# Performance work log

Hardware: AMD Instinct MI355X
Metric: run time of the kernel (lower is better)

## Reference

```python
import jax, jax.numpy as jnp
import numpy as np

B = 131072
UNITS = 256
INPUT_DIM = 256


def setup_inputs() -> dict:
    key = jax.random.key(0)
    ks = jax.random.split(key, 8)
    x = jax.random.normal(ks[0], (B, INPUT_DIM), dtype=jnp.float32)
    h_prev = jax.random.normal(ks[1], (B, UNITS), dtype=jnp.float32)
    c_prev = jax.random.normal(ks[2], (B, UNITS), dtype=jnp.float32)
    # glorot-like scale for W: fan_in = INPUT_DIM + UNITS, fan_out = 4*UNITS
    scale = jnp.sqrt(2.0 / (INPUT_DIM + UNITS + 4 * UNITS)).astype(jnp.float32)
    W = jax.random.normal(ks[3], (INPUT_DIM + UNITS, 4 * UNITS), dtype=jnp.float32) * scale
    # bias: zeros except forget gate initialized to 1.0
    b = jnp.concatenate([
        jnp.zeros(UNITS, jnp.float32),
        jnp.ones(UNITS, jnp.float32),
        jnp.zeros(UNITS, jnp.float32),
        jnp.zeros(UNITS, jnp.float32),
    ])
    peephole_i = jax.random.normal(ks[4], (UNITS,), dtype=jnp.float32) * 0.05
    peephole_f = jax.random.normal(ks[5], (UNITS,), dtype=jnp.float32) * 0.05
    peephole_o = jax.random.normal(ks[6], (UNITS,), dtype=jnp.float32) * 0.05
    return {
        "x": x, "h_prev": h_prev, "c_prev": c_prev,
        "W": W, "b": b,
        "peephole_i": peephole_i, "peephole_f": peephole_f, "peephole_o": peephole_o,
    }


def reference(x, h_prev, c_prev, W, b, peephole_i, peephole_f, peephole_o):
    combined = jnp.concatenate([x, h_prev], axis=-1)          # [B, INPUT_DIM+UNITS]
    z = combined @ W + b                                      # [B, 4*UNITS]
    i, f, c_hat, o = jnp.split(z, 4, axis=1)                  # each [B, UNITS]
    i = jax.nn.sigmoid(i + peephole_i * c_prev)
    f = jax.nn.sigmoid(f + peephole_f * c_prev)
    o = jax.nn.sigmoid(o + peephole_o * c_prev)
    c_hat = jnp.tanh(c_hat)
    c = f * c_prev + i * c_hat
    h = o * jnp.tanh(c)
    return (h, h, c)  # matches (output, [h, c]) of the Keras cell
```

## Files before the change

kernel.cpp:

```cpp
#include <hip/hip_runtime.h>
#include <cstdint>

#define NROWS   131072
#define NUNITS  256
#define KTOT    512
#define BM      256
#define THREADS 512

typedef float f32x4  __attribute__((ext_vector_type(4)));
typedef short bf16x8 __attribute__((ext_vector_type(8)));

__device__ __forceinline__ short f2bf(float x) {
    unsigned u = __float_as_uint(x);
    u += 0x7FFFu + ((u >> 16) & 1u);
    return (short)(u >> 16);
}

__global__ void convert_kernel(const float* __restrict__ x, const float* __restrict__ h,
                               const float* __restrict__ W,
                               short* __restrict__ Aws, short* __restrict__ Wws) {
    int b = blockIdx.x;
    if (b < 32768) {
        int i = b * 256 + threadIdx.x;
        int row = i >> 6;
        int c   = (i & 63) * 4;
        float4 xv = *(const float4*)(x + (size_t)row * 256 + c);
        float4 hv = *(const float4*)(h + (size_t)row * 256 + c);
        short xs[4] = {f2bf(xv.x), f2bf(xv.y), f2bf(xv.z), f2bf(xv.w)};
        short hs[4] = {f2bf(hv.x), f2bf(hv.y), f2bf(hv.z), f2bf(hv.w)};
        *(uint2*)(Aws + (size_t)row * 512 + c)       = *(uint2*)xs;
        *(uint2*)(Aws + (size_t)row * 512 + 256 + c) = *(uint2*)hs;
    } else {
        int i = (b - 32768) * 256 + threadIdx.x;
        int k = i >> 10;
        int c = i & 1023;
        Wws[((size_t)(k >> 5) << 15) + ((size_t)c << 5) + (k & 31)] = f2bf(W[i]);
    }
}

__global__ void __launch_bounds__(THREADS, 2)
lstm_main_kernel(const float* __restrict__ c_prev, const float* __restrict__ bias,
                 const float* __restrict__ pi, const float* __restrict__ pf,
                 const float* __restrict__ po, const short* __restrict__ Aws,
                 const short* __restrict__ Wws, float* __restrict__ out) {
    __shared__ short lds[2][32768];

    const int bid = blockIdx.x;
    const int swz = (bid & 7) * 256 + (bid >> 3);
    const int ut  = swz & 3;
    const int rt  = swz >> 2;
    const int row0 = rt * BM;

    const int t    = threadIdx.x;
    const int lane = t & 63;
    const int w    = t >> 6;
    const int lr   = lane & 15;
    const int hi   = lane >> 4;
    const int rh   = w >> 2;
    const int q    = w & 3;

    const short* srcA[2];
    const short* srcB[2];
    #pragma unroll
    for (int rep = 0; rep < 2; ++rep) {
        const int G    = rep * 512 + t;
        const int arow = G >> 2, ag = G & 3;
        srcA[rep] = Aws + (size_t)(row0 + arow) * 512 + ((ag ^ ((arow >> 1) & 3)) * 8);
        const int cp = G >> 2, bg = G & 3;
        const int gate = cp >> 6, u64 = cp & 63;
        srcB[rep] = Wws + (size_t)(gate * 256 + ut * 64 + u64) * 32
                        + ((bg ^ ((cp >> 1) & 3)) * 8);
    }

    const int sw    = (hi ^ ((lr >> 1) & 3)) * 8;
    const int abase = (rh * 128 + lr) * 32 + sw;
    const int bbase = 16384 + (q * 16 + lr) * 32 + sw;

    f32x4 acc[8][4];
    #pragma unroll
    for (int m = 0; m < 8; ++m)
        #pragma unroll
        for (int g = 0; g < 4; ++g)
            acc[m][g] = (f32x4){0.f, 0.f, 0.f, 0.f};

    auto dma = [&](int kt, int buf) {
        short* base = &lds[buf][0];
        #pragma unroll
        for (int rep = 0; rep < 2; ++rep)
            #pragma unroll
            for (int kk = 0; kk < 2; ++kk) {
                __builtin_amdgcn_global_load_lds(
                    (const __attribute__((address_space(1))) uint32_t*)(const void*)
                        (srcA[rep] + kt * 64 + kk * 32),
                    (__attribute__((address_space(3))) uint32_t*)(void*)
                        (base + kk * 8192 + (rep * 512 + t) * 8), 16, 0, 0);
                __builtin_amdgcn_global_load_lds(
                    (const __attribute__((address_space(1))) uint32_t*)(const void*)
                        (srcB[rep] + (size_t)(kt * 2 + kk) * 32768),
                    (__attribute__((address_space(3))) uint32_t*)(void*)
                        (base + 16384 + kk * 8192 + (rep * 512 + t) * 8), 16, 0, 0);
            }
    };

    auto compute = [&](int buf) {
        const short* L = &lds[buf][0];
        #pragma unroll
        for (int kk = 0; kk < 2; ++kk) {
            bf16x8 bfr[4], af[8];
            #pragma unroll
            for (int g = 0; g < 4; ++g)
                bfr[g] = *(const bf16x8*)&L[bbase + kk * 8192 + g * 2048];
            #pragma unroll
            for (int m = 0; m < 8; ++m)
                af[m] = *(const bf16x8*)&L[abase + kk * 8192 + m * 512];
            __builtin_amdgcn_s_setprio(1);
            #pragma unroll
            for (int g = 0; g < 4; ++g)
                #pragma unroll
                for (int m = 0; m < 8; ++m)
                    acc[m][g] = __builtin_amdgcn_mfma_f32_16x16x32_bf16(af[m], bfr[g], acc[m][g], 0, 0, 0);
            __builtin_amdgcn_s_setprio(0);
        }
    };

    dma(0, 0);
    #pragma unroll 1
    for (int kt = 0; kt < 8; ++kt) {
        asm volatile("s_waitcnt vmcnt(0)" ::: "memory");
        __builtin_amdgcn_s_barrier();
        if (kt < 7) dma(kt + 1, (kt + 1) & 1);
        compute(kt & 1);
    }

    const size_t HS = (size_t)NROWS * NUNITS;
    const int u = ut * 64 + q * 16 + lr;
    const float bi = bias[u],       bfg = bias[256 + u];
    const float bc = bias[512 + u], bo  = bias[768 + u];
    const float ppi = pi[u], ppf = pf[u], ppo = po[u];
    #pragma unroll
    for (int m = 0; m < 8; ++m) {
        #pragma unroll
        for (int r = 0; r < 4; ++r) {
            const int row = row0 + rh * 128 + m * 16 + hi * 4 + r;
            const size_t o = (size_t)row * NUNITS + u;
            const float cp = c_prev[o];
            float zi = acc[m][0][r] + bi  + ppi * cp;
            float zf = acc[m][1][r] + bfg + ppf * cp;
            float zc = acc[m][2][r] + bc;
            float zo = acc[m][3][r] + bo  + ppo * cp;
            float ig = 1.f / (1.f + __expf(-zi));
            float fg = 1.f / (1.f + __expf(-zf));
            float og = 1.f / (1.f + __expf(-zo));
            zc = fminf(fmaxf(zc, -30.f), 30.f);
            float e2 = __expf(2.f * zc);
            float chat = (e2 - 1.f) / (e2 + 1.f);
            float c  = fg * cp + ig * chat;
            float ccl = fminf(fmaxf(c, -30.f), 30.f);
            float e3 = __expf(2.f * ccl);
            float th = (e3 - 1.f) / (e3 + 1.f);
            float h  = og * th;
            out[o]          = h;
            out[HS + o]     = h;
            out[2 * HS + o] = c;
        }
    }
}

extern "C" void kernel_launch(void* const* d_in, const int* in_sizes, int n_in,
                              void* d_out, int out_size, void* d_ws, size_t ws_size,
                              hipStream_t stream) {
    const float* x  = (const float*)d_in[0];
    const float* h  = (const float*)d_in[1];
    const float* c  = (const float*)d_in[2];
    const float* W  = (const float*)d_in[3];
    const float* b  = (const float*)d_in[4];
    const float* pi = (const float*)d_in[5];
    const float* pf = (const float*)d_in[6];
    const float* po = (const float*)d_in[7];
    float* out = (float*)d_out;

    const size_t aws_bytes = (size_t)NROWS * KTOT * 2;
    short* Aws = (short*)d_ws;
    short* Wws = (short*)((char*)d_ws + aws_bytes);

    hipLaunchKernelGGL(convert_kernel, dim3(32768 + 2048), dim3(256), 0, stream,
                       x, h, W, Aws, Wws);
    hipLaunchKernelGGL(lstm_main_kernel, dim3(NROWS / BM * 4), dim3(THREADS), 0, stream,
                       c, b, pi, pf, po, Aws, Wws, out);
}
```

Baseline: 350.8 us.

## Deepen GEMM K pipeline to four smaller LDS stages with partial waitcnt

Splits the K loop into 16 stages of 32 instead of 8 stages of 64, and cycles through 4 LDS buffers. Three loads stay in flight, and the wait uses vmcnt(8) rather than draining all loads. The goal is to hide global-to-LDS load latency behind MFMA work, in place of the old double buffer that waited on every load. In exchange there are twice as many barriers, each with less compute per stage. The buffer-reuse order also needs correct vmcnt accounting.

```diff
diff --git a/kernel.cpp b/kernel.cpp
--- a/kernel.cpp
+++ b/kernel.cpp
@@ -43,7 +43,7 @@
                  const float* __restrict__ pi, const float* __restrict__ pf,
                  const float* __restrict__ po, const short* __restrict__ Aws,
                  const short* __restrict__ Wws, float* __restrict__ out) {
-    __shared__ short lds[2][32768];
+    __shared__ short lds[4][16384];
 
     const int bid = blockIdx.x;
     const int swz = (bid & 7) * 256 + (bid >> 3);
@@ -59,22 +59,17 @@
     const int rh   = w >> 2;
     const int q    = w & 3;
 
-    const short* srcA[2];
-    const short* srcB[2];
-    #pragma unroll
-    for (int rep = 0; rep < 2; ++rep) {
-        const int G    = rep * 512 + t;
-        const int arow = G >> 2, ag = G & 3;
-        srcA[rep] = Aws + (size_t)(row0 + arow) * 512 + ((ag ^ ((arow >> 1) & 3)) * 8);
-        const int cp = G >> 2, bg = G & 3;
-        const int gate = cp >> 6, u64 = cp & 63;
-        srcB[rep] = Wws + (size_t)(gate * 256 + ut * 64 + u64) * 32
-                        + ((bg ^ ((cp >> 1) & 3)) * 8);
-    }
+    const int arow = t >> 2, aslot = t & 3;
+    const short* srcA0 = Aws + (size_t)(row0 + arow) * 512
+                             + ((aslot ^ ((arow >> 1) & 3)) * 8);
+    const int bcol = t >> 2, bslot = t & 3;
+    const int gate0 = bcol >> 6, u64c = bcol & 63;
+    const short* srcB0 = Wws + (size_t)(gate0 * 256 + ut * 64 + u64c) * 32
+                             + ((bslot ^ ((bcol >> 1) & 3)) * 8);
 
-    const int sw    = (hi ^ ((lr >> 1) & 3)) * 8;
-    const int abase = (rh * 128 + lr) * 32 + sw;
-    const int bbase = 16384 + (q * 16 + lr) * 32 + sw;
+    const int sw   = (hi ^ ((lr >> 1) & 3)) * 8;
+    const int aoff = (rh * 128 + lr) * 32 + sw;
+    const int boff = 8192 + (q * 16 + lr) * 32 + sw;
 
     f32x4 acc[8][4];
     #pragma unroll
@@ -83,54 +78,59 @@
         for (int g = 0; g < 4; ++g)
             acc[m][g] = (f32x4){0.f, 0.f, 0.f, 0.f};
 
-    auto dma = [&](int kt, int buf) {
-        short* base = &lds[buf][0];
-        #pragma unroll
-        for (int rep = 0; rep < 2; ++rep)
-            #pragma unroll
-            for (int kk = 0; kk < 2; ++kk) {
-                __builtin_amdgcn_global_load_lds(
-                    (const __attribute__((address_space(1))) uint32_t*)(const void*)
-                        (srcA[rep] + kt * 64 + kk * 32),
-                    (__attribute__((address_space(3))) uint32_t*)(void*)
-                        (base + kk * 8192 + (rep * 512 + t) * 8), 16, 0, 0);
-                __builtin_amdgcn_global_load_lds(
-                    (const __attribute__((address_space(1))) uint32_t*)(const void*)
-                        (srcB[rep] + (size_t)(kt * 2 + kk) * 32768),
-                    (__attribute__((address_space(3))) uint32_t*)(void*)
-                        (base + 16384 + kk * 8192 + (rep * 512 + t) * 8), 16, 0, 0);
-            }
+    auto dma = [&](int ks, int buf) {
+        short* dst = &lds[buf][0];
+        const short* a0 = srcA0 + ks * 32;
+        const short* b0 = srcB0 + (size_t)ks * 32768;
+        __builtin_amdgcn_global_load_lds(
+            (const __attribute__((address_space(1))) uint32_t*)(const void*)a0,
+            (__attribute__((address_space(3))) uint32_t*)(void*)(dst + t * 8), 16, 0, 0);
+        __builtin_amdgcn_global_load_lds(
+            (const __attribute__((address_space(1))) uint32_t*)(const void*)(a0 + 65536),
+            (__attribute__((address_space(3))) uint32_t*)(void*)(dst + 4096 + t * 8), 16, 0, 0);
+        __builtin_amdgcn_global_load_lds(
+            (const __attribute__((address_space(1))) uint32_t*)(const void*)b0,
+            (__attribute__((address_space(3))) uint32_t*)(void*)(dst + 8192 + t * 8), 16, 0, 0);
+        __builtin_amdgcn_global_load_lds(
+            (const __attribute__((address_space(1))) uint32_t*)(const void*)(b0 + 16384),
+            (__attribute__((address_space(3))) uint32_t*)(void*)(dst + 12288 + t * 8), 16, 0, 0);
     };
 
     auto compute = [&](int buf) {
         const short* L = &lds[buf][0];
+        bf16x8 bfr[4], af[8];
         #pragma unroll
-        for (int kk = 0; kk < 2; ++kk) {
-            bf16x8 bfr[4], af[8];
-            #pragma unroll
-            for (int g = 0; g < 4; ++g)
-                bfr[g] = *(const bf16x8*)&L[bbase + kk * 8192 + g * 2048];
+        for (int g = 0; g < 4; ++g)
+            bfr[g] = *(const bf16x8*)&L[boff + g * 2048];
+        #pragma unroll
+        for (int m = 0; m < 8; ++m)
+            af[m] = *(const bf16x8*)&L[aoff + m * 512];
+        __builtin_amdgcn_s_setprio(1);
+        #pragma unroll
+        for (int g = 0; g < 4; ++g)
             #pragma unroll
             for (int m = 0; m < 8; ++m)
-                af[m] = *(const bf16x8*)&L[abase + kk * 8192 + m * 512];
-            __builtin_amdgcn_s_setprio(1);
-            #pragma unroll
-            for (int g = 0; g < 4; ++g)
-                #pragma unroll
-                for (int m = 0; m < 8; ++m)
-                    acc[m][g] = __builtin_amdgcn_mfma_f32_16x16x32_bf16(af[m], bfr[g], acc[m][g], 0, 0, 0);
-            __builtin_amdgcn_s_setprio(0);
-        }
+                acc[m][g] = __builtin_amdgcn_mfma_f32_16x16x32_bf16(af[m], bfr[g], acc[m][g], 0, 0, 0);
+        __builtin_amdgcn_s_setprio(0);
     };
 
     dma(0, 0);
+    dma(1, 1);
+    dma(2, 2);
+
     #pragma unroll 1
-    for (int kt = 0; kt < 8; ++kt) {
-        asm volatile("s_waitcnt vmcnt(0)" ::: "memory");
+    for (int p = 0; p < 14; ++p) {
+        asm volatile("s_waitcnt vmcnt(8)" ::: "memory");
         __builtin_amdgcn_s_barrier();
-        if (kt < 7) dma(kt + 1, (kt + 1) & 1);
-        compute(kt & 1);
+        if (p <= 12) dma(p + 3, (p + 3) & 3);
+        compute(p & 3);
     }
+    asm volatile("s_waitcnt vmcnt(4)" ::: "memory");
+    __builtin_amdgcn_s_barrier();
+    compute(2);
+    asm volatile("s_waitcnt vmcnt(0)" ::: "memory");
+    __builtin_amdgcn_s_barrier();
+    compute(3);
 
     const size_t HS = (size_t)NROWS * NUNITS;
     const int u = ut * 64 + q * 16 + lr;
```

Result: faster. 338.2 us (-3.6%).
